# Kernel tuning notes

Measured on AMD Instinct MI355X. Metric: run time of the kernel, lower is better.

The kernel has to match this reference:

```python
import jax, jax.numpy as jnp
import numpy as np

ALPHA = 0.15
EPSILON = 0.01
RHO = 1e-4
NUM_ITERS = 20  # fixed-iteration unrolling of the data-dependent while-loop (see notes)
N_NODES = 100_000
N_EDGES = 1_600_000
N_SEEDS = 8


def setup_inputs() -> dict:
    rng = np.random.default_rng(0)
    row = rng.integers(0, N_NODES, N_EDGES).astype(np.int32)
    row[:N_NODES] = np.arange(N_NODES, dtype=np.int32)  # every node has >= 1 out-edge
    col = rng.integers(0, N_NODES, N_EDGES).astype(np.int32)
    val = np.ones(N_EDGES, dtype=np.float32)
    deg = np.bincount(row, minlength=N_NODES).astype(np.float32)
    seeds = rng.integers(0, N_NODES, N_SEEDS).astype(np.int32)
    return {
        "adj_row": jnp.asarray(row),
        "adj_col": jnp.asarray(col),
        "adj_val": jnp.asarray(val),
        "out_degree": jnp.asarray(deg),
        "seeds": jnp.asarray(seeds),
    }


def reference(adj_row, adj_col, adj_val, out_degree, seeds):
    n = out_degree.shape[0]
    deg_inv = 1.0 / jnp.maximum(out_degree, 1e-12)
    thresh = (1.0 + EPSILON) * RHO * ALPHA
    half = 0.5 * (1.0 - ALPHA) * deg_inv  # 0.5*(1-alpha)/deg, precomputed [n]

    def single(seed):
        p0 = jnp.zeros((n,), jnp.float32)
        d0 = jnp.zeros((n,), jnp.float32).at[seed].set(-ALPHA * deg_inv[seed])

        def body(carry, _):
            p, d = carry
            active = jnp.max(jnp.abs(d)) > thresh  # while-loop condition
            S = (p - d) >= RHO * ALPHA              # active frontier S_k
            d_pk = jnp.where(S, -(d + RHO * ALPHA), 0.0)  # is_d_pk (zero off S_k)
            # per-edge push: row r gathers v*d_pk[c] / (v*S[c]*deg[c] + 1e-12)
            num = adj_val * d_pk[adj_col]
            den = adj_val * jnp.where(S[adj_col], out_degree[adj_col], 0.0) + 1e-12
            tmp = jax.ops.segment_sum(num / den, adj_row, num_segments=n)
            d_S = (1.0 - deg_inv) * d - RHO * ALPHA * deg_inv - half * d_pk - half * tmp
            d_nb = d - half * tmp  # neighbor update (tmp==0 for non-neighbors)
            d_new = jnp.where(S, d_S, d_nb)
            p_new = jnp.where(S, p + d_pk, p)
            p2 = jnp.where(active, p_new, p)
            d2 = jnp.where(active, d_new, d)
            return (p2, d2), None

        (p, _), _ = jax.lax.scan(body, (p0, d0), None, length=NUM_ITERS)
        return p

    # dense PPR vectors per seed node [N_SEEDS, n] (the torch module returns their nonzero supports)
    return jax.vmap(single)(seeds)
```

## Files before the change

### kernel.cpp

```cpp
#include <hip/hip_runtime.h>

#define ALPHA   0.15f
#define RA      (1e-4f * 0.15f)
#define THRESH  ((1.0f + 0.01f) * 1e-4f * 0.15f)
#define NITER   20
#define NS      8
#define NMIR    64
#define CHW     32
#define BLK     256
#define W4      (BLK / 64)
#define SPAN    768
#define NBIN    8
#define ECHUNK  2048
#define NWMAX   3136

__global__ void init_kernel(const float* __restrict__ deg, const int* __restrict__ seeds,
                            float2* __restrict__ pd, float* __restrict__ dpw,
                            int* __restrict__ cursor, int* __restrict__ flagM,
                            unsigned* __restrict__ maskA, int N) {
    int idx = blockIdx.x * blockDim.x + threadIdx.x;
    int NW = (N + 31) >> 5;
    if (idx < (NITER + 1) * NMIR) {
        int v = 0;
        if (idx == 0) {
            for (int s = 0; s < NS; ++s) {
                float m = ALPHA / fmaxf(deg[seeds[s]], 1e-12f);
                if (m > THRESH) v |= (1 << s);
            }
        }
        flagM[idx] = v;
    }
    if (idx < NW) {
        unsigned v = 0;
        for (int s = 0; s < NS; ++s) {
            int sd = seeds[s];
            bool S0 = (ALPHA / fmaxf(deg[sd], 1e-12f)) >= RA;
            if (S0 && (sd >> 5) == idx) v |= (1u << (sd & 31));
        }
        maskA[idx] = v;
    }
    if (idx >= N) return;
    cursor[idx] = 0;
    float dv[NS];
#pragma unroll
    for (int s = 0; s < NS; ++s) dv[s] = 0.f;
#pragma unroll
    for (int s = 0; s < NS; ++s) {
        if (seeds[s] == idx) dv[s] = -ALPHA / fmaxf(deg[idx], 1e-12f);
    }
    float den = deg[idx] + 1e-12f;
#pragma unroll
    for (int s = 0; s < NS; ++s) {
        pd[idx * NS + s] = make_float2(0.f, dv[s]);
        bool S = (0.f - dv[s]) >= RA;
        dpw[idx * NS + s] = S ? (-(dv[s] + RA) / den) : 0.f;
    }
}

__global__ void block_sum_kernel(const float* __restrict__ deg, int* __restrict__ blockSums, int N) {
    int i = blockIdx.x * 256 + threadIdx.x;
    int v = (i < N) ? (int)deg[i] : 0;
#pragma unroll
    for (int o = 1; o < 64; o <<= 1) v += __shfl_xor(v, o);
    __shared__ int ws[4];
    if ((threadIdx.x & 63) == 0) ws[threadIdx.x >> 6] = v;
    __syncthreads();
    if (threadIdx.x == 0) blockSums[blockIdx.x] = ws[0] + ws[1] + ws[2] + ws[3];
}

__global__ void scan_sums_kernel(const int* __restrict__ blockSums, int* __restrict__ blockOffs, int nB) {
    __shared__ int buf[1024];
    int t = threadIdx.x;
    int v = (t < nB) ? blockSums[t] : 0;
    buf[t] = v;
    __syncthreads();
    for (int o = 1; o < 1024; o <<= 1) {
        int u = (t >= o) ? buf[t - o] : 0;
        __syncthreads();
        buf[t] += u;
        __syncthreads();
    }
    if (t < nB) blockOffs[t] = buf[t] - v;
}

__global__ void write_offs_kernel(const float* __restrict__ deg, const int* __restrict__ blockOffs,
                                  int* __restrict__ offs, int N, int E) {
    int t = threadIdx.x;
    int i = blockIdx.x * 256 + t;
    int v = (i < N) ? (int)deg[i] : 0;
    __shared__ int buf[256];
    buf[t] = v;
    __syncthreads();
    for (int o = 1; o < 256; o <<= 1) {
        int u = (t >= o) ? buf[t - o] : 0;
        __syncthreads();
        buf[t] += u;
        __syncthreads();
    }
    int excl = buf[t] - v;
    if (i < N) offs[i] = blockOffs[blockIdx.x] + excl;
    if (i == 0) offs[N] = E;
}

__global__ void scatter_kernel(const int* __restrict__ row, const int* __restrict__ col,
                               const int* __restrict__ offs, int* __restrict__ cursor,
                               int* __restrict__ cols, int E, int N) {
    int bin = blockIdx.x & (NBIN - 1);
    int chunk = blockIdx.x >> 3;
    int binW = (N + NBIN - 1) / NBIN;
    int binLo = bin * binW;
    int binHi = min(N, binLo + binW);
    int e = chunk * ECHUNK + threadIdx.x;
#pragma unroll
    for (int i = 0; i < ECHUNK / 256; ++i, e += 256) {
        if (e < E) {
            int r = row[e];
            if (r >= binLo && r < binHi) {
                int pos = offs[r] + atomicAdd(&cursor[r], 1);
                cols[pos] = col[e];
            }
        }
    }
}

__global__ __launch_bounds__(BLK, 4) void update_kernel(
        const int* __restrict__ offs, const int* __restrict__ cols,
        const float* __restrict__ deg,
        const int* __restrict__ flagIn, int* __restrict__ flagOut,
        const unsigned* __restrict__ maskIn, unsigned* __restrict__ maskOut,
        const float* __restrict__ din, float* __restrict__ dout,
        float2* __restrict__ pd, float* __restrict__ outp, int last, int N) {
    __shared__ unsigned smask[NWMAX];
    __shared__ int sColsAll[W4 * SPAN];
    int tid = threadIdx.x;
    int w = tid >> 6;
    int lane = tid & 63;
    int wid = blockIdx.x * W4 + w;
    int base = wid * CHW;
    int NW = (N + 31) >> 5;
    int* sCols = sColsAll + w * SPAN;

    int r  = lane >> 1;
    int sh = lane & 1;
    int row = base + r;
    bool rok = row < N;

    int fm = flagIn[lane];
#pragma unroll
    for (int o = 1; o < 64; o <<= 1) fm |= __shfl_xor(fm, o);

    if (fm == 0) {
        if (last && rok) {
            const float4* pp = (const float4*)(pd + (size_t)row * NS + 4 * sh);
            float4 A = pp[0], B = pp[1];
            outp[(4 * sh + 0) * (size_t)N + row] = A.x;
            outp[(4 * sh + 1) * (size_t)N + row] = A.z;
            outp[(4 * sh + 2) * (size_t)N + row] = B.x;
            outp[(4 * sh + 3) * (size_t)N + row] = B.z;
        }
        return;
    }

    for (int i = tid; i < NW; i += BLK) smask[i] = maskIn[i];
    __syncthreads();

    int offv = 0;
    if (lane <= CHW) offv = offs[min(base + lane, N)];
    int off0 = __shfl(offv, 0);
    int span = __shfl(offv, CHW) - off0;
    int e0 = __shfl(offv, r);
    int e1 = __shfl(offv, r + 1);
    int rel = e0 - off0, ndg = e1 - e0;

    bool fits = (span <= SPAN);
    if (fits) {
        for (int i = lane; i < span; i += 64) {
            int cc = cols[off0 + i];
            sCols[i] = ((smask[cc >> 5] >> (cc & 31)) & 1u) ? cc : -1;
        }
    }

    int mx = ndg;
#pragma unroll
    for (int o = 1; o < 64; o <<= 1) mx = max(mx, __shfl_xor(mx, o));

    float a0 = 0.f, a1 = 0.f, a2 = 0.f, a3 = 0.f;
    const float4* din4 = (const float4*)din;
    if (fits) {
#pragma unroll 4
        for (int i = 0; i < mx; ++i) {
            int idx = (i < ndg) ? (rel + i) : 0;
            int cc = sCols[idx];
            if (i < ndg && cc >= 0) {
                float4 v = din4[(size_t)cc * 2 + sh];
                a0 += v.x; a1 += v.y; a2 += v.z; a3 += v.w;
            }
        }
    } else {
        for (int i = 0; i < mx; ++i) {
            if (i < ndg) {
                int cc = cols[e0 + i];
                if ((smask[cc >> 5] >> (cc & 31)) & 1u) {
                    float4 v = din4[(size_t)cc * 2 + sh];
                    a0 += v.x; a1 += v.y; a2 += v.z; a3 += v.w;
                }
            }
        }
    }

    float dg = 1.0f;
    if (rok) dg = deg[row];
    float di = 1.0f / fmaxf(dg, 1e-12f);
    float hf = 0.5f * (1.0f - ALPHA) * di;
    float den = dg + 1e-12f;

    float4 pdA = make_float4(0.f, 0.f, 0.f, 0.f), pdB = pdA;
    if (rok) {
        const float4* pp = (const float4*)(pd + (size_t)row * NS + 4 * sh);
        pdA = pp[0]; pdB = pp[1];
    }
    float p0 = pdA.x, d0 = pdA.y, p1 = pdA.z, d1 = pdA.w;
    float p2v = pdB.x, d2v = pdB.y, p3 = pdB.z, d3 = pdB.w;
    float w0, w1, w2, w3;
    unsigned fireN = 0, nzN = 0;
    bool chg = false;

#define UPD(PK, DK, AK, K, WK) { \
        bool S = (PK - DK) >= RA; \
        float dpkv = S ? -(DK + RA) : 0.f; \
        float dS  = (1.0f - di) * DK - RA * di - hf * dpkv - hf * AK; \
        float dnb = DK - hf * AK; \
        bool aa = (fm >> (4 * sh + K)) & 1; \
        float nd2 = aa ? (S ? dS : dnb) : DK; \
        float np2 = aa ? (S ? PK + dpkv : PK) : PK; \
        bool S2 = (np2 - nd2) >= RA; \
        WK = S2 ? (-(nd2 + RA) / den) : 0.f; \
        if (aa && (S || AK != 0.f)) chg = true; \
        if (aa && fabsf(nd2) > THRESH) fireN |= 1u << K; \
        if (WK != 0.f) nzN |= 1u << K; \
        PK = np2; DK = nd2; }
    UPD(p0, d0, a0, 0, w0)
    UPD(p1, d1, a1, 1, w1)
    UPD(p2v, d2v, a2, 2, w2)
    UPD(p3, d3, a3, 3, w3)
#undef UPD

    if (last) {
        if (rok) {
            outp[(4 * sh + 0) * (size_t)N + row] = p0;
            outp[(4 * sh + 1) * (size_t)N + row] = p1;
            outp[(4 * sh + 2) * (size_t)N + row] = p2v;
            outp[(4 * sh + 3) * (size_t)N + row] = p3;
        }
    } else {
        int nzl = (nzN != 0) ? 1 : 0;
        int rn = nzl | __shfl_xor(nzl, 1);
        if (rok && chg) {
            float4* pp = (float4*)(pd + (size_t)row * NS + 4 * sh);
            pp[0] = make_float4(p0, d0, p1, d1);
            pp[1] = make_float4(p2v, d2v, p3, d3);
        }
        if (rok && rn) {
            *(float4*)(dout + (size_t)row * NS + 4 * sh) = make_float4(w0, w1, w2, w3);
        }
        int rnv = __shfl(rn, (lane & 31) * 2);
        unsigned long long bw = __ballot(lane < 32 && rnv);
        if (lane == 0 && wid < NW) maskOut[wid] = (unsigned)bw;

        int wm = 0;
#pragma unroll
        for (int b = 0; b < 4; ++b) {
            unsigned long long bb = __ballot((fireN >> b) & 1);
            if (bb & 0x5555555555555555ull) wm |= 1 << b;
            if (bb & 0xAAAAAAAAAAAAAAAAull) wm |= 1 << (4 + b);
        }
        if (wm && lane == 0) {
            int hsh = wid & (NMIR - 1);
            int cur = __hip_atomic_load(&flagOut[hsh], __ATOMIC_RELAXED,
                                        __HIP_MEMORY_SCOPE_AGENT);
            if ((cur & wm) != wm) atomicOr(&flagOut[hsh], wm);
        }
    }
}

extern "C" void kernel_launch(void* const* d_in, const int* in_sizes, int n_in,
                              void* d_out, int out_size, void* d_ws, size_t ws_size,
                              hipStream_t stream) {
    const int*   adj_row = (const int*)  d_in[0];
    const int*   adj_col = (const int*)  d_in[1];
    const float* deg     = (const float*)d_in[3];
    const int*   seeds   = (const int*)  d_in[4];
    const int E = in_sizes[0];
    const int N = in_sizes[3];
    float* out = (float*)d_out;

    char* base = (char*)d_ws;
    size_t off = 0;
    auto carve = [&](size_t bytes) -> void* {
        off = (off + 255) & ~(size_t)255;
        void* ptr = base + off;
        off += bytes;
        return ptr;
    };
    float2*   pd     = (float2*)  carve((size_t)N * NS * 8);
    float*    dpwB   = (float*)   carve((size_t)N * NS * 4);
    int*      cols   = (int*)     carve((size_t)(E + SPAN) * 4);
    int*      offs   = (int*)     carve((size_t)(N + 1) * 4);
    int*      cursor = (int*)     carve((size_t)N * 4);
    int*      bsums  = (int*)     carve((size_t)1024 * 4);
    int*      boffs  = (int*)     carve((size_t)1024 * 4);
    int*      flagM  = (int*)     carve((size_t)(NITER + 1) * NMIR * 4);
    unsigned* maskA  = (unsigned*)carve((size_t)NWMAX * 4);
    unsigned* maskB  = (unsigned*)carve((size_t)NWMAX * 4);
    float*    dpwA   = out;

    int nb = (N + 255) / 256;
    init_kernel<<<nb, 256, 0, stream>>>(deg, seeds, pd, dpwA, cursor, flagM, maskA, N);
    block_sum_kernel<<<nb, 256, 0, stream>>>(deg, bsums, N);
    scan_sums_kernel<<<1, 1024, 0, stream>>>(bsums, boffs, nb);
    write_offs_kernel<<<nb, 256, 0, stream>>>(deg, boffs, offs, N, E);
    int chunks = (E + ECHUNK - 1) / ECHUNK;
    scatter_kernel<<<chunks * NBIN, 256, 0, stream>>>(adj_row, adj_col, offs, cursor,
                                                      cols, E, N);

    float*    din   = dpwA;
    float*    dout_ = dpwB;
    unsigned* mIn   = maskA;
    unsigned* mOut  = maskB;
    int rowsPerBlk = W4 * CHW;
    int ub = (N + rowsPerBlk - 1) / rowsPerBlk;
    for (int k = 0; k < NITER; ++k) {
        int last = (k == NITER - 1) ? 1 : 0;
        update_kernel<<<ub, BLK, 0, stream>>>(offs, cols, deg,
                                              flagM + k * NMIR, flagM + (k + 1) * NMIR,
                                              mIn, mOut, din, dout_, pd, out, last, N);
        float* t = din; din = dout_; dout_ = t;
        unsigned* mt = mIn; mIn = mOut; mOut = mt;
    }
}
```

Baseline: 379.4 us.

## Use four lanes per row with float2 gathers and fuse block-sum into init

The update kernel now assigns four lanes per row, each handling two seeds with float2 gathers, instead of two lanes per row handling four seeds with float4. Each wavefront covers 16 rows rather than 32, so the shared column span halves and launch bounds rise to allow more resident blocks. The active-row mask word is now assembled across two wavefronts through shared memory and a block barrier. The separate block-sum kernel is folded into init to save a launch, at the cost of more thread blocks and narrower memory transactions per gather.

```diff
diff --git a/kernel.cpp b/kernel.cpp
--- a/kernel.cpp
+++ b/kernel.cpp
@@ -6,10 +6,10 @@
 #define NITER   20
 #define NS      8
 #define NMIR    64
-#define CHW     32
+#define CHW     16
 #define BLK     256
 #define W4      (BLK / 64)
-#define SPAN    768
+#define SPAN    384
 #define NBIN    8
 #define ECHUNK  2048
 #define NWMAX   3136
@@ -17,55 +17,54 @@
 __global__ void init_kernel(const float* __restrict__ deg, const int* __restrict__ seeds,
                             float2* __restrict__ pd, float* __restrict__ dpw,
                             int* __restrict__ cursor, int* __restrict__ flagM,
-                            unsigned* __restrict__ maskA, int N) {
+                            unsigned* __restrict__ maskA, int* __restrict__ blockSums,
+                            int N) {
     int idx = blockIdx.x * blockDim.x + threadIdx.x;
     int NW = (N + 31) >> 5;
-    if (idx < (NITER + 1) * NMIR) {
-        int v = 0;
-        if (idx == 0) {
-            for (int s = 0; s < NS; ++s) {
-                float m = ALPHA / fmaxf(deg[seeds[s]], 1e-12f);
-                if (m > THRESH) v |= (1 << s);
-            }
-        }
-        flagM[idx] = v;
-    }
-    if (idx < NW) {
-        unsigned v = 0;
-        for (int s = 0; s < NS; ++s) {
-            int sd = seeds[s];
-            bool S0 = (ALPHA / fmaxf(deg[sd], 1e-12f)) >= RA;
-            if (S0 && (sd >> 5) == idx) v |= (1u << (sd & 31));
-        }
-        maskA[idx] = v;
-    }
-    if (idx >= N) return;
-    cursor[idx] = 0;
-    float dv[NS];
-#pragma unroll
-    for (int s = 0; s < NS; ++s) dv[s] = 0.f;
-#pragma unroll
-    for (int s = 0; s < NS; ++s) {
-        if (seeds[s] == idx) dv[s] = -ALPHA / fmaxf(deg[idx], 1e-12f);
-    }
-    float den = deg[idx] + 1e-12f;
-#pragma unroll
-    for (int s = 0; s < NS; ++s) {
-        pd[idx * NS + s] = make_float2(0.f, dv[s]);
-        bool S = (0.f - dv[s]) >= RA;
-        dpw[idx * NS + s] = S ? (-(dv[s] + RA) / den) : 0.f;
-    }
-}
-
-__global__ void block_sum_kernel(const float* __restrict__ deg, int* __restrict__ blockSums, int N) {
-    int i = blockIdx.x * 256 + threadIdx.x;
-    int v = (i < N) ? (int)deg[i] : 0;
+
+    int v = (idx < N) ? (int)deg[idx] : 0;
 #pragma unroll
     for (int o = 1; o < 64; o <<= 1) v += __shfl_xor(v, o);
     __shared__ int ws[4];
     if ((threadIdx.x & 63) == 0) ws[threadIdx.x >> 6] = v;
     __syncthreads();
     if (threadIdx.x == 0) blockSums[blockIdx.x] = ws[0] + ws[1] + ws[2] + ws[3];
+
+    if (idx < (NITER + 1) * NMIR) {
+        int fv = 0;
+        if (idx == 0) {
+            for (int s = 0; s < NS; ++s) {
+                float m = ALPHA / fmaxf(deg[seeds[s]], 1e-12f);
+                if (m > THRESH) fv |= (1 << s);
+            }
+        }
+        flagM[idx] = fv;
+    }
+    if (idx < NW) {
+        unsigned mv = 0;
+        for (int s = 0; s < NS; ++s) {
+            int sd = seeds[s];
+            bool S0 = (ALPHA / fmaxf(deg[sd], 1e-12f)) >= RA;
+            if (S0 && (sd >> 5) == idx) mv |= (1u << (sd & 31));
+        }
+        maskA[idx] = mv;
+    }
+    if (idx >= N) return;
+    cursor[idx] = 0;
+    float dv[NS];
+#pragma unroll
+    for (int s = 0; s < NS; ++s) dv[s] = 0.f;
+#pragma unroll
+    for (int s = 0; s < NS; ++s) {
+        if (seeds[s] == idx) dv[s] = -ALPHA / fmaxf(deg[idx], 1e-12f);
+    }
+    float den = deg[idx] + 1e-12f;
+#pragma unroll
+    for (int s = 0; s < NS; ++s) {
+        pd[idx * NS + s] = make_float2(0.f, dv[s]);
+        bool S = (0.f - dv[s]) >= RA;
+        dpw[idx * NS + s] = S ? (-(dv[s] + RA) / den) : 0.f;
+    }
 }
 
 __global__ void scan_sums_kernel(const int* __restrict__ blockSums, int* __restrict__ blockOffs, int nB) {
@@ -123,7 +122,7 @@
     }
 }
 
-__global__ __launch_bounds__(BLK, 4) void update_kernel(
+__global__ __launch_bounds__(BLK, 6) void update_kernel(
         const int* __restrict__ offs, const int* __restrict__ cols,
         const float* __restrict__ deg,
         const int* __restrict__ flagIn, int* __restrict__ flagOut,
@@ -132,6 +131,7 @@
         float2* __restrict__ pd, float* __restrict__ outp, int last, int N) {
     __shared__ unsigned smask[NWMAX];
     __shared__ int sColsAll[W4 * SPAN];
+    __shared__ unsigned sRow[W4];
     int tid = threadIdx.x;
     int w = tid >> 6;
     int lane = tid & 63;
@@ -140,9 +140,9 @@
     int NW = (N + 31) >> 5;
     int* sCols = sColsAll + w * SPAN;
 
-    int r  = lane >> 1;
-    int sh = lane & 1;
-    int row = base + r;
+    int r4 = lane >> 2;
+    int q  = lane & 3;
+    int row = base + r4;
     bool rok = row < N;
 
     int fm = flagIn[lane];
@@ -151,12 +151,9 @@
 
     if (fm == 0) {
         if (last && rok) {
-            const float4* pp = (const float4*)(pd + (size_t)row * NS + 4 * sh);
-            float4 A = pp[0], B = pp[1];
-            outp[(4 * sh + 0) * (size_t)N + row] = A.x;
-            outp[(4 * sh + 1) * (size_t)N + row] = A.z;
-            outp[(4 * sh + 2) * (size_t)N + row] = B.x;
-            outp[(4 * sh + 3) * (size_t)N + row] = B.z;
+            float4 pv4 = ((const float4*)(pd + (size_t)row * NS))[q];
+            outp[(2 * q + 0) * (size_t)N + row] = pv4.x;
+            outp[(2 * q + 1) * (size_t)N + row] = pv4.z;
         }
         return;
     }
@@ -168,8 +165,8 @@
     if (lane <= CHW) offv = offs[min(base + lane, N)];
     int off0 = __shfl(offv, 0);
     int span = __shfl(offv, CHW) - off0;
-    int e0 = __shfl(offv, r);
-    int e1 = __shfl(offv, r + 1);
+    int e0 = __shfl(offv, r4);
+    int e1 = __shfl(offv, r4 + 1);
     int rel = e0 - off0, ndg = e1 - e0;
 
     bool fits = (span <= SPAN);
@@ -184,16 +181,22 @@
 #pragma unroll
     for (int o = 1; o < 64; o <<= 1) mx = max(mx, __shfl_xor(mx, o));
 
-    float a0 = 0.f, a1 = 0.f, a2 = 0.f, a3 = 0.f;
-    const float4* din4 = (const float4*)din;
+    float dg = 1.0f;
+    float4 pdv = make_float4(0.f, 0.f, 0.f, 0.f);
+    if (rok) {
+        dg = deg[row];
+        pdv = ((const float4*)(pd + (size_t)row * NS))[q];
+    }
+
+    float a0 = 0.f, a1 = 0.f;
+    const float2* din2 = (const float2*)din;
     if (fits) {
-#pragma unroll 4
+#pragma unroll 8
         for (int i = 0; i < mx; ++i) {
-            int idx = (i < ndg) ? (rel + i) : 0;
-            int cc = sCols[idx];
-            if (i < ndg && cc >= 0) {
-                float4 v = din4[(size_t)cc * 2 + sh];
-                a0 += v.x; a1 += v.y; a2 += v.z; a3 += v.w;
+            int cc = (i < ndg) ? sCols[rel + i] : -1;
+            if (cc >= 0) {
+                float2 v = din2[(size_t)cc * 4 + q];
+                a0 += v.x; a1 += v.y;
             }
         }
     } else {
@@ -201,78 +204,72 @@
             if (i < ndg) {
                 int cc = cols[e0 + i];
                 if ((smask[cc >> 5] >> (cc & 31)) & 1u) {
-                    float4 v = din4[(size_t)cc * 2 + sh];
-                    a0 += v.x; a1 += v.y; a2 += v.z; a3 += v.w;
+                    float2 v = din2[(size_t)cc * 4 + q];
+                    a0 += v.x; a1 += v.y;
                 }
             }
         }
     }
 
-    float dg = 1.0f;
-    if (rok) dg = deg[row];
     float di = 1.0f / fmaxf(dg, 1e-12f);
     float hf = 0.5f * (1.0f - ALPHA) * di;
     float den = dg + 1e-12f;
 
-    float4 pdA = make_float4(0.f, 0.f, 0.f, 0.f), pdB = pdA;
-    if (rok) {
-        const float4* pp = (const float4*)(pd + (size_t)row * NS + 4 * sh);
-        pdA = pp[0]; pdB = pp[1];
-    }
-    float p0 = pdA.x, d0 = pdA.y, p1 = pdA.z, d1 = pdA.w;
-    float p2v = pdB.x, d2v = pdB.y, p3 = pdB.z, d3 = pdB.w;
-    float w0, w1, w2, w3;
+    float p0 = pdv.x, d0 = pdv.y, p1 = pdv.z, d1 = pdv.w;
+    float w0, w1;
     unsigned fireN = 0, nzN = 0;
     bool chg = false;
 
-#define UPD(PK, DK, AK, K, WK) { \
+#define UPD(PK, DK, AK, B, WK) { \
         bool S = (PK - DK) >= RA; \
         float dpkv = S ? -(DK + RA) : 0.f; \
         float dS  = (1.0f - di) * DK - RA * di - hf * dpkv - hf * AK; \
         float dnb = DK - hf * AK; \
-        bool aa = (fm >> (4 * sh + K)) & 1; \
+        bool aa = (fm >> (2 * q + B)) & 1; \
         float nd2 = aa ? (S ? dS : dnb) : DK; \
         float np2 = aa ? (S ? PK + dpkv : PK) : PK; \
         bool S2 = (np2 - nd2) >= RA; \
         WK = S2 ? (-(nd2 + RA) / den) : 0.f; \
         if (aa && (S || AK != 0.f)) chg = true; \
-        if (aa && fabsf(nd2) > THRESH) fireN |= 1u << K; \
-        if (WK != 0.f) nzN |= 1u << K; \
+        if (aa && fabsf(nd2) > THRESH) fireN |= 1u << B; \
+        if (WK != 0.f) nzN |= 1u << B; \
         PK = np2; DK = nd2; }
     UPD(p0, d0, a0, 0, w0)
     UPD(p1, d1, a1, 1, w1)
-    UPD(p2v, d2v, a2, 2, w2)
-    UPD(p3, d3, a3, 3, w3)
 #undef UPD
 
     if (last) {
         if (rok) {
-            outp[(4 * sh + 0) * (size_t)N + row] = p0;
-            outp[(4 * sh + 1) * (size_t)N + row] = p1;
-            outp[(4 * sh + 2) * (size_t)N + row] = p2v;
-            outp[(4 * sh + 3) * (size_t)N + row] = p3;
+            outp[(2 * q + 0) * (size_t)N + row] = p0;
+            outp[(2 * q + 1) * (size_t)N + row] = p1;
         }
     } else {
         int nzl = (nzN != 0) ? 1 : 0;
-        int rn = nzl | __shfl_xor(nzl, 1);
+        nzl |= __shfl_xor(nzl, 1);
+        nzl |= __shfl_xor(nzl, 2);
         if (rok && chg) {
-            float4* pp = (float4*)(pd + (size_t)row * NS + 4 * sh);
-            pp[0] = make_float4(p0, d0, p1, d1);
-            pp[1] = make_float4(p2v, d2v, p3, d3);
-        }
-        if (rok && rn) {
-            *(float4*)(dout + (size_t)row * NS + 4 * sh) = make_float4(w0, w1, w2, w3);
-        }
-        int rnv = __shfl(rn, (lane & 31) * 2);
-        unsigned long long bw = __ballot(lane < 32 && rnv);
-        if (lane == 0 && wid < NW) maskOut[wid] = (unsigned)bw;
+            ((float4*)(pd + (size_t)row * NS))[q] = make_float4(p0, d0, p1, d1);
+        }
+        if (rok && nzl) {
+            ((float2*)(dout + (size_t)row * NS))[q] = make_float2(w0, w1);
+        }
+        int rnv = __shfl(nzl, (lane & 15) * 4);
+        unsigned long long bw = __ballot(lane < 16 && rnv);
+        if (lane == 0) sRow[w] = (unsigned)(bw & 0xFFFFull);
+        __syncthreads();
+        if (tid < 2) {
+            unsigned wv = sRow[2 * tid] | (sRow[2 * tid + 1] << 16);
+            int word = blockIdx.x * 2 + tid;
+            if (word < NW) maskOut[word] = wv;
+        }
 
         int wm = 0;
-#pragma unroll
-        for (int b = 0; b < 4; ++b) {
-            unsigned long long bb = __ballot((fireN >> b) & 1);
-            if (bb & 0x5555555555555555ull) wm |= 1 << b;
-            if (bb & 0xAAAAAAAAAAAAAAAAull) wm |= 1 << (4 + b);
+        unsigned long long bb0 = __ballot(fireN & 1);
+        unsigned long long bb1 = __ballot((fireN >> 1) & 1);
+#pragma unroll
+        for (int qq = 0; qq < 4; ++qq) {
+            if (bb0 & (0x1111111111111111ull << qq)) wm |= 1 << (2 * qq);
+            if (bb1 & (0x1111111111111111ull << qq)) wm |= 1 << (2 * qq + 1);
         }
         if (wm && lane == 0) {
             int hsh = wid & (NMIR - 1);
@@ -315,8 +312,8 @@
     float*    dpwA   = out;
 
     int nb = (N + 255) / 256;
-    init_kernel<<<nb, 256, 0, stream>>>(deg, seeds, pd, dpwA, cursor, flagM, maskA, N);
-    block_sum_kernel<<<nb, 256, 0, stream>>>(deg, bsums, N);
+    init_kernel<<<nb, 256, 0, stream>>>(deg, seeds, pd, dpwA, cursor, flagM, maskA,
+                                        bsums, N);
     scan_sums_kernel<<<1, 1024, 0, stream>>>(bsums, boffs, nb);
     write_offs_kernel<<<nb, 256, 0, stream>>>(deg, boffs, offs, N, E);
     int chunks = (E + ECHUNK - 1) / ECHUNK;
```

After: 370.7 us. 1.02x faster.
